# Optimization experiments

Measured on AMD Instinct MI355X. Metric: run time of the kernel, lower is better.

The kernel has to match this reference:

```python
import jax, jax.numpy as jnp
import numpy as np

KH, KW = 5, 5            # local window (h, w), must be odd
SIGMA = 1.0
GAUSS_DEN = 2.0 * SIGMA ** 2
N, C, H, W = 4, 20, 64, 2048


def setup_inputs() -> dict:
    key = jax.random.key(0)
    k1, k2, k3 = jax.random.split(key, 3)
    xyz = jax.random.normal(k1, (N, 3, H, W), dtype=jnp.float32)
    softmax = jax.random.uniform(k2, (N, C, H, W), dtype=jnp.float32)
    mask = jax.random.randint(k3, (N, H, W), 0, 2).astype(jnp.bool_)
    return {"xyz": xyz, "softmax": softmax, "mask": mask}


def reference(xyz, softmax, mask):
    # xyz: [N,3,H,W], softmax: [N,C,H,W], mask: [N,H,W]
    sm = softmax * mask[:, None].astype(softmax.dtype)
    ph, pw = KH // 2, KW // 2
    # zero padding matches F.unfold's implicit zero padding
    xyz_p = jnp.pad(xyz, ((0, 0), (0, 0), (ph, ph), (pw, pw)))
    sm_p = jnp.pad(sm, ((0, 0), (0, 0), (ph, ph), (pw, pw)))
    out = jnp.zeros_like(sm)
    # Fused form of the im2col math: for each window offset, weight the
    # shifted (masked) softmax by the XYZ-distance Gaussian and accumulate.
    # 25 static offsets -> small fixed unrolled loop, no giant unfold buffers.
    for dy in range(KH):
        for dx in range(KW):
            wxyz = xyz_p[:, :, dy:dy + sm.shape[2], dx:dx + sm.shape[3]]  # [N,3,H,W]
            d2 = jnp.sum((wxyz - xyz) ** 2, axis=1)                       # [N,H,W]
            g = jnp.exp(-d2 / GAUSS_DEN)                                  # [N,H,W]
            out = out + g[:, None] * sm_p[:, :, dy:dy + sm.shape[2], dx:dx + sm.shape[3]]
    return out
```

## Files before the change

kernel.cpp:

```cpp
#include <hip/hip_runtime.h>

#define NN 4
#define CC 20
#define HH 64
#define WW 2048
#define CG 2
#define CPG (CC / CG)
#define PX 4

__global__ __launch_bounds__(256, 4) void lc_xyz_kernel(
    const float* __restrict__ xyz,
    const float* __restrict__ softmax,
    const int* __restrict__ mask,
    float* __restrict__ out)
{
    const int t  = blockIdx.x * blockDim.x + threadIdx.x;
    const int h  = blockIdx.y;
    const int nz = blockIdx.z;
    const int n  = nz >> 1;
    const int cg = nz & 1;
    const int hw = HH * WW;
    const int p0 = t * PX;

    const float* xb  = xyz     + (size_t)n * 3  * hw;
    const float* smb = softmax + (size_t)n * CC * hw + (size_t)(cg * CPG) * hw;
    const int*   mb  = mask    + (size_t)n * hw;

    const int ctr = h * WW + p0;
    const float4 cxv = *(const float4*)(xb + 0 * hw + ctr);
    const float4 cyv = *(const float4*)(xb + 1 * hw + ctr);
    const float4 czv = *(const float4*)(xb + 2 * hw + ctr);
    const float cx[PX] = {cxv.x, cxv.y, cxv.z, cxv.w};
    const float cy[PX] = {cyv.x, cyv.y, cyv.z, cyv.w};
    const float cz[PX] = {czv.x, czv.y, czv.z, czv.w};

    float acc[CPG][PX];
#pragma unroll
    for (int c = 0; c < CPG; ++c)
#pragma unroll
        for (int i = 0; i < PX; ++i) acc[c][i] = 0.f;

    int c0 = p0 - 4; if (c0 < 0) c0 = 0;
    const int c1 = p0;
    int c2 = p0 + 4; if (c2 > WW - 4) c2 = WW - 4;

    float vf[12];
#pragma unroll
    for (int j = 2; j <= 9; ++j)
        vf[j] = ((unsigned)(p0 - 4 + j) < (unsigned)WW) ? 1.f : 0.f;

#pragma unroll
    for (int dy = -2; dy <= 2; ++dy) {
        const int row = h + dy;
        if ((unsigned)row >= (unsigned)HH) continue;
        const int rb = row * WW;

        const int4 m0 = *(const int4*)(mb + rb + c0);
        const int4 m1 = *(const int4*)(mb + rb + c1);
        const int4 m2 = *(const int4*)(mb + rb + c2);
        const float4 x0 = *(const float4*)(xb + 0 * hw + rb + c0);
        const float4 x1 = *(const float4*)(xb + 0 * hw + rb + c1);
        const float4 x2 = *(const float4*)(xb + 0 * hw + rb + c2);
        const float4 y0 = *(const float4*)(xb + 1 * hw + rb + c0);
        const float4 y1 = *(const float4*)(xb + 1 * hw + rb + c1);
        const float4 y2 = *(const float4*)(xb + 1 * hw + rb + c2);
        const float4 z0 = *(const float4*)(xb + 2 * hw + rb + c0);
        const float4 z1 = *(const float4*)(xb + 2 * hw + rb + c1);
        const float4 z2 = *(const float4*)(xb + 2 * hw + rb + c2);

        const float xw[12] = {x0.x,x0.y,x0.z,x0.w, x1.x,x1.y,x1.z,x1.w, x2.x,x2.y,x2.z,x2.w};
        const float yw[12] = {y0.x,y0.y,y0.z,y0.w, y1.x,y1.y,y1.z,y1.w, y2.x,y2.y,y2.z,y2.w};
        const float zw[12] = {z0.x,z0.y,z0.z,z0.w, z1.x,z1.y,z1.z,z1.w, z2.x,z2.y,z2.z,z2.w};
        const int   mi[12] = {m0.x,m0.y,m0.z,m0.w, m1.x,m1.y,m1.z,m1.w, m2.x,m2.y,m2.z,m2.w};

        float mf[12];
#pragma unroll
        for (int j = 2; j <= 9; ++j) mf[j] = vf[j] * (float)mi[j];

        float g[PX][5];
#pragma unroll
        for (int i = 0; i < PX; ++i) {
#pragma unroll
            for (int dx = 0; dx < 5; ++dx) {
                const int j = i + dx + 2;
                const float ax = xw[j] - cx[i];
                const float ay = yw[j] - cy[i];
                const float az = zw[j] - cz[i];
                const float d2 = ax * ax + ay * ay + az * az;
                g[i][dx] = mf[j] * __expf(-0.5f * d2);
            }
        }

#pragma unroll
        for (int c = 0; c < CPG; ++c) {
            const float* sp = smb + (size_t)c * hw + rb;
            const float4 s0 = *(const float4*)(sp + c0);
            const float4 s1 = *(const float4*)(sp + c1);
            const float4 s2 = *(const float4*)(sp + c2);
            const float sw[12] = {s0.x,s0.y,s0.z,s0.w, s1.x,s1.y,s1.z,s1.w, s2.x,s2.y,s2.z,s2.w};
#pragma unroll
            for (int i = 0; i < PX; ++i) {
                float a = acc[c][i];
#pragma unroll
                for (int dx = 0; dx < 5; ++dx)
                    a = fmaf(g[i][dx], sw[i + dx + 2], a);
                acc[c][i] = a;
            }
        }
    }

    float* ob = out + (size_t)n * CC * hw + (size_t)(cg * CPG) * hw + ctr;
#pragma unroll
    for (int c = 0; c < CPG; ++c)
        *(float4*)(ob + (size_t)c * hw) =
            make_float4(acc[c][0], acc[c][1], acc[c][2], acc[c][3]);
}

extern "C" void kernel_launch(void* const* d_in, const int* in_sizes, int n_in,
                              void* d_out, int out_size, void* d_ws, size_t ws_size,
                              hipStream_t stream) {
    const float* xyz     = (const float*)d_in[0];
    const float* softmax = (const float*)d_in[1];
    const int*   mask    = (const int*)d_in[2];
    float*       out     = (float*)d_out;

    dim3 block(256, 1, 1);
    dim3 grid(WW / (PX * 256), HH, NN * CG);
    hipLaunchKernelGGL(lc_xyz_kernel, grid, block, 0, stream,
                       xyz, softmax, mask, out);
}
```

Before: 153.7 us.

## Share Gaussian weights across channel teams via LDS with 1024-thread blocks

Blocks grow to 1024 threads covering 1024 pixels of one row, split into four teams of five channels each. Each row's xyz and mask halo is staged in shared memory and each thread computes the 5 Gaussian weights for one pixel into LDS once. All four channel teams then read these weights, so no exp is computed twice across channel groups. This costs two __syncthreads per window row, a less unrolled row loop, and lower occupancy flexibility with large blocks.

```diff
diff --git a/kernel.cpp b/kernel.cpp
--- a/kernel.cpp
+++ b/kernel.cpp
@@ -4,114 +4,131 @@
 #define CC 20
 #define HH 64
 #define WW 2048
-#define CG 2
-#define CPG (CC / CG)
-#define PX 4
+#define TEAMS 4
+#define CPT 5
+#define BPX 1024
+#define NQ 256
+#define HALO 1032
+#define GSTR 21
 
-__global__ __launch_bounds__(256, 4) void lc_xyz_kernel(
+__global__ __launch_bounds__(1024, 4) void lc_xyz_kernel(
     const float* __restrict__ xyz,
     const float* __restrict__ softmax,
     const int* __restrict__ mask,
     float* __restrict__ out)
 {
-    const int t  = blockIdx.x * blockDim.x + threadIdx.x;
-    const int h  = blockIdx.y;
-    const int nz = blockIdx.z;
-    const int n  = nz >> 1;
-    const int cg = nz & 1;
-    const int hw = HH * WW;
-    const int p0 = t * PX;
+    __shared__ float ls_x[HALO];
+    __shared__ float ls_y[HALO];
+    __shared__ float ls_z[HALO];
+    __shared__ float ls_m[HALO];
+    __shared__ float gq[NQ * GSTR];
+
+    const int tid = (int)threadIdx.x;
+    const int w0  = (int)blockIdx.x * BPX;
+    const int h   = (int)blockIdx.y;
+    const int n   = (int)blockIdx.z;
+    const int hw  = HH * WW;
 
     const float* xb  = xyz     + (size_t)n * 3  * hw;
-    const float* smb = softmax + (size_t)n * CC * hw + (size_t)(cg * CPG) * hw;
+    const float* smb = softmax + (size_t)n * CC * hw + (size_t)((tid >> 8) * CPT) * hw;
     const int*   mb  = mask    + (size_t)n * hw;
 
-    const int ctr = h * WW + p0;
-    const float4 cxv = *(const float4*)(xb + 0 * hw + ctr);
-    const float4 cyv = *(const float4*)(xb + 1 * hw + ctr);
-    const float4 czv = *(const float4*)(xb + 2 * hw + ctr);
-    const float cx[PX] = {cxv.x, cxv.y, cxv.z, cxv.w};
-    const float cy[PX] = {cyv.x, cyv.y, cyv.z, cyv.w};
-    const float cz[PX] = {czv.x, czv.y, czv.z, czv.w};
+    const int pg   = tid;
+    const int pcen = w0 + pg;
+    const float cx = xb[0 * hw + h * WW + pcen];
+    const float cy = xb[1 * hw + h * WW + pcen];
+    const float cz = xb[2 * hw + h * WW + pcen];
 
-    float acc[CPG][PX];
+    const int q   = tid & 255;
+    const int p0q = w0 + 4 * q;
+    int c0 = p0q - 4; if (c0 < 0) c0 = 0;
+    const int c1 = p0q;
+    int c2 = p0q + 4; if (c2 > WW - 4) c2 = WW - 4;
+
+    float acc[CPT][4];
 #pragma unroll
-    for (int c = 0; c < CPG; ++c)
+    for (int c = 0; c < CPT; ++c)
 #pragma unroll
-        for (int i = 0; i < PX; ++i) acc[c][i] = 0.f;
+        for (int i = 0; i < 4; ++i) acc[c][i] = 0.f;
 
-    int c0 = p0 - 4; if (c0 < 0) c0 = 0;
-    const int c1 = p0;
-    int c2 = p0 + 4; if (c2 > WW - 4) c2 = WW - 4;
+    for (int r = 0; r < 5; ++r) {
+        const int  row  = h + r - 2;
+        const bool rval = (unsigned)row < (unsigned)HH;
+        const int  rowc = row < 0 ? 0 : (row > HH - 1 ? HH - 1 : row);
+        const int  rb   = rowc * WW;
 
-    float vf[12];
+        {
+            const int s  = tid;
+            const int w  = w0 - 4 + s;
+            const int wc = w < 0 ? 0 : (w > WW - 1 ? WW - 1 : w);
+            const float mv = (rval && (unsigned)w < (unsigned)WW)
+                                 ? (float)mb[rb + wc] : 0.f;
+            ls_x[s] = xb[0 * hw + rb + wc];
+            ls_y[s] = xb[1 * hw + rb + wc];
+            ls_z[s] = xb[2 * hw + rb + wc];
+            ls_m[s] = mv;
+        }
+        if (tid < HALO - BPX) {
+            const int s  = BPX + tid;
+            const int w  = w0 - 4 + s;
+            const int wc = w > WW - 1 ? WW - 1 : w;
+            const float mv = (rval && (unsigned)w < (unsigned)WW)
+                                 ? (float)mb[rb + wc] : 0.f;
+            ls_x[s] = xb[0 * hw + rb + wc];
+            ls_y[s] = xb[1 * hw + rb + wc];
+            ls_z[s] = xb[2 * hw + rb + wc];
+            ls_m[s] = mv;
+        }
+        __syncthreads();
+
+        {
+            const int gb = (pg >> 2) * GSTR + (pg & 3) * 5;
 #pragma unroll
-    for (int j = 2; j <= 9; ++j)
-        vf[j] = ((unsigned)(p0 - 4 + j) < (unsigned)WW) ? 1.f : 0.f;
+            for (int d = 0; d < 5; ++d) {
+                const int s = pg + 2 + d;
+                const float ax = ls_x[s] - cx;
+                const float ay = ls_y[s] - cy;
+                const float az = ls_z[s] - cz;
+                const float d2 = ax * ax + ay * ay + az * az;
+                gq[gb + d] = ls_m[s] * __expf(-0.5f * d2);
+            }
+        }
+        __syncthreads();
+
+        {
+            float g[4][5];
+            const int gb = q * GSTR;
+#pragma unroll
+            for (int i = 0; i < 4; ++i)
+#pragma unroll
+                for (int d = 0; d < 5; ++d)
+                    g[i][d] = gq[gb + i * 5 + d];
 
 #pragma unroll
-    for (int dy = -2; dy <= 2; ++dy) {
-        const int row = h + dy;
-        if ((unsigned)row >= (unsigned)HH) continue;
-        const int rb = row * WW;
-
-        const int4 m0 = *(const int4*)(mb + rb + c0);
-        const int4 m1 = *(const int4*)(mb + rb + c1);
-        const int4 m2 = *(const int4*)(mb + rb + c2);
-        const float4 x0 = *(const float4*)(xb + 0 * hw + rb + c0);
-        const float4 x1 = *(const float4*)(xb + 0 * hw + rb + c1);
-        const float4 x2 = *(const float4*)(xb + 0 * hw + rb + c2);
-        const float4 y0 = *(const float4*)(xb + 1 * hw + rb + c0);
-        const float4 y1 = *(const float4*)(xb + 1 * hw + rb + c1);
-        const float4 y2 = *(const float4*)(xb + 1 * hw + rb + c2);
-        const float4 z0 = *(const float4*)(xb + 2 * hw + rb + c0);
-        const float4 z1 = *(const float4*)(xb + 2 * hw + rb + c1);
-        const float4 z2 = *(const float4*)(xb + 2 * hw + rb + c2);
-
-        const float xw[12] = {x0.x,x0.y,x0.z,x0.w, x1.x,x1.y,x1.z,x1.w, x2.x,x2.y,x2.z,x2.w};
-        const float yw[12] = {y0.x,y0.y,y0.z,y0.w, y1.x,y1.y,y1.z,y1.w, y2.x,y2.y,y2.z,y2.w};
-        const float zw[12] = {z0.x,z0.y,z0.z,z0.w, z1.x,z1.y,z1.z,z1.w, z2.x,z2.y,z2.z,z2.w};
-        const int   mi[12] = {m0.x,m0.y,m0.z,m0.w, m1.x,m1.y,m1.z,m1.w, m2.x,m2.y,m2.z,m2.w};
-
-        float mf[12];
+            for (int c = 0; c < CPT; ++c) {
+                const float* sp = smb + (size_t)c * hw + rb;
+                const float4 s0 = *(const float4*)(sp + c0);
+                const float4 s1 = *(const float4*)(sp + c1);
+                const float4 s2 = *(const float4*)(sp + c2);
+                const float sw[12] = {s0.x,s0.y,s0.z,s0.w,
+                                      s1.x,s1.y,s1.z,s1.w,
+                                      s2.x,s2.y,s2.z,s2.w};
 #pragma unroll
-        for (int j = 2; j <= 9; ++j) mf[j] = vf[j] * (float)mi[j];
-
-        float g[PX][5];
+                for (int i = 0; i < 4; ++i) {
+                    float a = acc[c][i];
 #pragma unroll
-        for (int i = 0; i < PX; ++i) {
-#pragma unroll
-            for (int dx = 0; dx < 5; ++dx) {
-                const int j = i + dx + 2;
-                const float ax = xw[j] - cx[i];
-                const float ay = yw[j] - cy[i];
-                const float az = zw[j] - cz[i];
-                const float d2 = ax * ax + ay * ay + az * az;
-                g[i][dx] = mf[j] * __expf(-0.5f * d2);
-            }
-        }
-
-#pragma unroll
-        for (int c = 0; c < CPG; ++c) {
-            const float* sp = smb + (size_t)c * hw + rb;
-            const float4 s0 = *(const float4*)(sp + c0);
-            const float4 s1 = *(const float4*)(sp + c1);
-            const float4 s2 = *(const float4*)(sp + c2);
-            const float sw[12] = {s0.x,s0.y,s0.z,s0.w, s1.x,s1.y,s1.z,s1.w, s2.x,s2.y,s2.z,s2.w};
-#pragma unroll
-            for (int i = 0; i < PX; ++i) {
-                float a = acc[c][i];
-#pragma unroll
-                for (int dx = 0; dx < 5; ++dx)
-                    a = fmaf(g[i][dx], sw[i + dx + 2], a);
-                acc[c][i] = a;
+                    for (int d = 0; d < 5; ++d)
+                        a = fmaf(g[i][d], sw[i + d + 2], a);
+                    acc[c][i] = a;
+                }
             }
         }
     }
 
-    float* ob = out + (size_t)n * CC * hw + (size_t)(cg * CPG) * hw + ctr;
+    float* ob = out + (size_t)n * CC * hw + (size_t)((tid >> 8) * CPT) * hw
+              + (size_t)h * WW + p0q;
 #pragma unroll
-    for (int c = 0; c < CPG; ++c)
+    for (int c = 0; c < CPT; ++c)
         *(float4*)(ob + (size_t)c * hw) =
             make_float4(acc[c][0], acc[c][1], acc[c][2], acc[c][3]);
 }
@@ -124,8 +141,8 @@
     const int*   mask    = (const int*)d_in[2];
     float*       out     = (float*)d_out;
 
-    dim3 block(256, 1, 1);
-    dim3 grid(WW / (PX * 256), HH, NN * CG);
+    dim3 block(1024, 1, 1);
+    dim3 grid(WW / BPX, HH, NN);
     hipLaunchKernelGGL(lc_xyz_kernel, grid, block, 0, stream,
                        xyz, softmax, mask, out);
 }
```

Result: slower. 323.8 us (+110.7%).
